# Kernel optimization log

Hardware: AMD Instinct MI355X
Metric: run time of the kernel (lower is better)

The kernel has to match this reference:

```python
import jax, jax.numpy as jnp
import numpy as np
from jax import lax

EPS = 1e-5


def _conv(x, w, b, stride, pad):
    # x: [B,C,H,W], w: [O,I,kh,kw] (NCHW / OIHW, same as torch Conv2d)
    y = lax.conv_general_dilated(
        x, w, window_strides=stride,
        padding=[(pad[0], pad[0]), (pad[1], pad[1])],
        dimension_numbers=('NCHW', 'OIHW', 'NCHW'))
    return y + b[None, :, None, None]


def _bn(x, gamma, beta, mean, var):
    # BatchNorm2d in eval mode (running statistics)
    inv = gamma / jnp.sqrt(var + EPS)
    return x * inv[None, :, None, None] + (beta - mean * inv)[None, :, None, None]


def _mask_time(x, lens):
    # Vectorized replacement of the per-sample narrow/fill loop:
    # zero every time step >= lens[b] along the last axis.
    t = jnp.arange(x.shape[3])
    keep = (t[None, :] < lens[:, None]).astype(x.dtype)  # [B, W]
    return x * keep[:, None, None, :]


def _new_len(lens, kernel_w, stride_w, pad_w):
    # matches get_new_sequence_lengths for Conv2d with dilation 1
    return (lens + 2 * pad_w - (kernel_w - 1) - 1) // stride_w + 1


def _forward(inputs, seq_lengths,
             w1, b1, g1, be1, m1, v1,
             w2, b2, g2, be2, m2, v2):
    lens = seq_lengths.astype(jnp.int32)
    # layer 1: Conv2d(1,32,(41,11),(2,2),(20,5))
    x = _conv(inputs, w1, b1, (2, 2), (20, 5))
    lens = _new_len(lens, 11, 2, 5)
    x = _mask_time(x, lens)
    # BatchNorm2d(32) -> mask
    x = _mask_time(_bn(x, g1, be1, m1, v1), lens)
    # Hardtanh(0,20) -> mask
    x = _mask_time(jnp.clip(x, 0.0, 20.0), lens)
    # layer 2: Conv2d(32,32,(21,11),(2,1),(10,5))
    x = _conv(x, w2, b2, (2, 1), (10, 5))
    lens = _new_len(lens, 11, 1, 5)
    x = _mask_time(x, lens)
    x = _mask_time(_bn(x, g2, be2, m2, v2), lens)
    x = _mask_time(jnp.clip(x, 0.0, 20.0), lens)
    return x, lens


def setup_inputs() -> dict:
    key = jax.random.key(0)
    ks = jax.random.split(key, 8)
    inputs = jax.random.normal(ks[0], (32, 1, 161, 1024), dtype=jnp.float32)
    seq_lengths = jax.random.randint(ks[1], (32,), 1, 1024, dtype=jnp.int32)
    w1 = jax.random.normal(ks[2], (32, 1, 41, 11), dtype=jnp.float32) * 0.05
    b1 = jax.random.normal(ks[3], (32,), dtype=jnp.float32) * 0.05
    w2 = jax.random.normal(ks[4], (32, 32, 21, 11), dtype=jnp.float32) * 0.02
    b2 = jax.random.normal(ks[5], (32,), dtype=jnp.float32) * 0.05
    g1 = jnp.ones((32,), jnp.float32)
    be1 = jnp.zeros((32,), jnp.float32)
    m1 = jax.random.normal(ks[6], (32,), dtype=jnp.float32) * 0.1
    v1 = jnp.ones((32,), jnp.float32)
    g2 = jnp.ones((32,), jnp.float32)
    be2 = jnp.zeros((32,), jnp.float32)
    m2 = jax.random.normal(ks[7], (32,), dtype=jnp.float32) * 0.1
    v2 = jnp.ones((32,), jnp.float32)
    return {"inputs": inputs, "seq_lengths": seq_lengths,
            "w1": w1, "b1": b1, "g1": g1, "be1": be1, "m1": m1, "v1": v1,
            "w2": w2, "b2": b2, "g2": g2, "be2": be2, "m2": m2, "v2": v2}


def reference(inputs, seq_lengths, w1, b1, g1, be1, m1, v1,
              w2, b2, g2, be2, m2, v2):
    return _forward(inputs, seq_lengths, w1, b1, g1, be1, m1, v1,
                    w2, b2, g2, be2, m2, v2)
```

## Files before the change

kernel.cpp:

```cpp
#include <hip/hip_runtime.h>
#include <math.h>

#define B_    32
#define H_IN  161
#define W_IN  1024
#define C1_   32
#define H1_   81
#define W1_   512
#define C2_   32
#define H2_   41
#define W2_   512

#define OUT_X_SZ ((size_t)B_ * C2_ * H2_ * W2_)

#define WF2_B    0u
#define WF1_B    473088u
#define SCSH_B   515072u
#define LENS1_B  515584u
#define XG_B     515712u

#define WF2_N    236544
#define WF1_N    20992

typedef __bf16 v8bf __attribute__((ext_vector_type(8)));
typedef float v16f __attribute__((ext_vector_type(16)));

static __device__ __forceinline__ unsigned short f2bf(float f) {
    unsigned int u = __float_as_uint(f);
    unsigned int r = (u + 0x7fffu + ((u >> 16) & 1u)) >> 16;
    return (unsigned short)r;
}

__global__ void prep_kernel(const float* __restrict__ w1, const float* __restrict__ b1,
                            const float* __restrict__ g1, const float* __restrict__ be1,
                            const float* __restrict__ m1, const float* __restrict__ v1,
                            const float* __restrict__ w2, const float* __restrict__ b2,
                            const float* __restrict__ g2, const float* __restrict__ be2,
                            const float* __restrict__ m2, const float* __restrict__ v2,
                            const int* __restrict__ lens,
                            unsigned short* __restrict__ wf1, unsigned short* __restrict__ wf2,
                            float* __restrict__ scsh, int* __restrict__ lens1,
                            float* __restrict__ out_lens)
{
    const int i = blockIdx.x * blockDim.x + threadIdx.x;
    const int stride = gridDim.x * blockDim.x;

    for (int idx = i; idx < WF2_N; idx += stride) {
        int j  = idx & 7;
        int l  = (idx >> 3) & 63;
        int f  = idx >> 9;
        int ch = f & 1;
        int kwkh = f >> 1;
        int kw = kwkh % 11;
        int kh = kwkh / 11;
        int oc = l & 31;
        int c  = ch * 16 + ((l >> 5) << 3) + j;
        wf2[idx] = f2bf(w2[((oc * 32 + c) * 21 + kh) * 11 + kw]);
    }
    for (int idx = i; idx < WF1_N; idx += stride) {
        int j  = idx & 7;
        int l  = (idx >> 3) & 63;
        int kh = idx >> 9;
        int k  = ((l >> 5) << 3) + j;
        int oc = l & 31;
        wf1[idx] = (k < 11) ? f2bf(w1[oc * 451 + kh * 11 + k]) : (unsigned short)0;
    }
    if (i < 32) {
        float s1 = g1[i] / sqrtf(v1[i] + 1e-5f);
        scsh[i]      = s1;
        scsh[32 + i] = b1[i] * s1 + be1[i] - m1[i] * s1;
        float s2 = g2[i] / sqrtf(v2[i] + 1e-5f);
        scsh[64 + i] = s2;
        scsh[96 + i] = b2[i] * s2 + be2[i] - m2[i] * s2;
        int l1 = (lens[i] - 1) / 2 + 1;
        if (l1 > W1_) l1 = W1_;
        lens1[i] = l1;
        out_lens[i] = (float)l1;
    }
}

__global__ __launch_bounds__(256) void conv1_mfma(
    const float* __restrict__ x,
    const unsigned short* __restrict__ wf1,
    const float* __restrict__ scsh,
    const int* __restrict__ lens1,
    unsigned short* __restrict__ xg)
{
    const int t    = threadIdx.x;
    const int lane = t & 63;
    const int l31  = lane & 31;
    const int lhi  = lane >> 5;
    const int wv   = t >> 6;
    const int w0   = blockIdx.x * 256;
    const int h    = blockIdx.y;
    const int b    = blockIdx.z;

    __shared__ unsigned int srow[2][264];

    v16f acc0, acc1;
#pragma unroll
    for (int i = 0; i < 16; ++i) { acc0[i] = 0.f; acc1[i] = 0.f; }

    const int r0 = 2 * h - 20;
    const int cb = 2 * w0 - 5;
    const float* xb = x + (size_t)b * (H_IN * W_IN);

    const int dwbase = wv * 64 + l31 + 4 * lhi;

    {
        float a0 = 0.f, a1 = 0.f, c0v = 0.f, c1v = 0.f;
        if (r0 >= 0 && r0 < H_IN) {
            const float* src = xb + (size_t)r0 * W_IN;
            int c0 = cb + 2 * t;
            if ((unsigned)c0 < (unsigned)W_IN)       a0 = src[c0];
            if ((unsigned)(c0 + 1) < (unsigned)W_IN) a1 = src[c0 + 1];
            if (t < 7) {
                int c1 = cb + 2 * (256 + t);
                if ((unsigned)c1 < (unsigned)W_IN)       c0v = src[c1];
                if ((unsigned)(c1 + 1) < (unsigned)W_IN) c1v = src[c1 + 1];
            }
        }
        srow[0][t] = (unsigned int)f2bf(a0) | ((unsigned int)f2bf(a1) << 16);
        if (t < 7)
            srow[0][256 + t] = (unsigned int)f2bf(c0v) | ((unsigned int)f2bf(c1v) << 16);
    }
    __syncthreads();

    for (int kh = 0; kh < 41; ++kh) {
        const int p = kh & 1;
        const int rn = r0 + kh + 1;
        const bool rv = (kh < 40) && (rn >= 0) && (rn < H_IN);

        float a0 = 0.f, a1 = 0.f, c0v = 0.f, c1v = 0.f;
        if (rv) {
            const float* src = xb + (size_t)rn * W_IN;
            int c0 = cb + 2 * t;
            if ((unsigned)c0 < (unsigned)W_IN)       a0 = src[c0];
            if ((unsigned)(c0 + 1) < (unsigned)W_IN) a1 = src[c0 + 1];
            if (t < 7) {
                int c1 = cb + 2 * (256 + t);
                if ((unsigned)c1 < (unsigned)W_IN)       c0v = src[c1];
                if ((unsigned)(c1 + 1) < (unsigned)W_IN) c1v = src[c1 + 1];
            }
        }

        const int r = r0 + kh;
        if (r >= 0 && r < H_IN) {
            uint4 a_u = *((const uint4*)wf1 + kh * 32 + lane);
            v8bf a = __builtin_bit_cast(v8bf, a_u);
            const unsigned int* bp = &srow[p][0];
            {
                int dw = dwbase;
                uint4 bu;
                bu.x = bp[dw]; bu.y = bp[dw + 1]; bu.z = bp[dw + 2]; bu.w = bp[dw + 3];
                v8bf bb = __builtin_bit_cast(v8bf, bu);
                acc0 = __builtin_amdgcn_mfma_f32_32x32x16_bf16(a, bb, acc0, 0, 0, 0);
            }
            {
                int dw = dwbase + 32;
                uint4 bu;
                bu.x = bp[dw]; bu.y = bp[dw + 1]; bu.z = bp[dw + 2]; bu.w = bp[dw + 3];
                v8bf bb = __builtin_bit_cast(v8bf, bu);
                acc1 = __builtin_amdgcn_mfma_f32_32x32x16_bf16(a, bb, acc1, 0, 0, 0);
            }
        }

        if (rv) {
            srow[p ^ 1][t] = (unsigned int)f2bf(a0) | ((unsigned int)f2bf(a1) << 16);
            if (t < 7)
                srow[p ^ 1][256 + t] = (unsigned int)f2bf(c0v) | ((unsigned int)f2bf(c1v) << 16);
        }
        __syncthreads();
    }

    const int l1 = lens1[b];
#pragma unroll
    for (int nt = 0; nt < 2; ++nt) {
        const int w = w0 + wv * 64 + nt * 32 + l31;
        const bool keep = (w < l1);
        unsigned short* dp = xg + (((size_t)b * H1_ + h) * W1_ + w) * 32;
#pragma unroll
        for (int rq = 0; rq < 4; ++rq) {
            unsigned int wd[2];
#pragma unroll
            for (int d = 0; d < 2; ++d) {
                int rg = rq * 4 + d * 2;
                int oc = 8 * rq + 4 * lhi + d * 2;
                float av0 = (nt == 0) ? acc0[rg]     : acc1[rg];
                float av1 = (nt == 0) ? acc0[rg + 1] : acc1[rg + 1];
                float v0 = fminf(fmaxf(fmaf(av0, scsh[oc],     scsh[32 + oc]), 0.f), 20.f);
                float v1 = fminf(fmaxf(fmaf(av1, scsh[oc + 1], scsh[33 + oc]), 0.f), 20.f);
                if (!keep) { v0 = 0.f; v1 = 0.f; }
                wd[d] = (unsigned int)f2bf(v0) | ((unsigned int)f2bf(v1) << 16);
            }
            uint2 u; u.x = wd[0]; u.y = wd[1];
            *(uint2*)(dp + 8 * rq + 4 * lhi) = u;
        }
    }
}

#define C2BUF 17024

__global__ __launch_bounds__(128, 2) void conv2_mfma(
    const unsigned short* __restrict__ xg,
    const unsigned short* __restrict__ wf2,
    const float* __restrict__ scsh,
    const int* __restrict__ lens1,
    float* __restrict__ out)
{
    const int t    = threadIdx.x;
    const int lane = t & 63;
    const int l31  = lane & 31;
    const int lhi  = lane >> 5;
    const int wid  = t >> 6;

    const int id   = blockIdx.x;
    const int sid  = (id & 7) * 168 + (id >> 3);
    const int wblk = sid & 1;
    const int bh   = sid >> 1;
    const int hp   = bh % 21;
    const int b    = bh / 21;
    const int h0   = hp << 1;
    const bool h1v = (h0 + 1) < 41;

    __shared__ __align__(16) char sbuf[2 * C2BUF];

    const int w0B = wblk << 8;
    const unsigned short* xb = xg + (size_t)b * (H1_ * W1_ * 32);

    int srcoff[9], ldsoff[9];
    bool vld[9];
#pragma unroll
    for (int i = 0; i < 9; ++i) {
        int k   = t + i * 128;
        int pos = k >> 2;
        int sg  = k & 3;
        int wp  = w0B + pos - 5;
        vld[i]    = (k < 1064) && (wp >= 0) && (wp < W1_);
        srcoff[i] = wp * 64 + sg * 16;
        ldsoff[i] = pos * 64 + ((sg ^ ((pos >> 1) & 3)) << 4);
    }

    const int rlo = max(0, 2 * h0 - 10);
    const int rhi = min(80, 2 * h0 + 12);

    v16f acc[2][4];
#pragma unroll
    for (int hh = 0; hh < 2; ++hh)
#pragma unroll
        for (int mt = 0; mt < 4; ++mt)
#pragma unroll
            for (int q = 0; q < 16; ++q) acc[hh][mt][q] = 0.f;

    uint4 g[9];

#define C2_STAGE_LOAD(ROW)                                                   \
    {                                                                        \
        const char* xrow = (const char*)(xb + (size_t)(ROW) * (W1_ * 32));   \
        _Pragma("unroll")                                                    \
        for (int i = 0; i < 9; ++i) {                                        \
            g[i].x = g[i].y = g[i].z = g[i].w = 0u;                          \
            if (vld[i]) g[i] = *(const uint4*)(xrow + srcoff[i]);            \
        }                                                                    \
    }

#define C2_STAGE_WRITE(PP)                                                   \
    {                                                                        \
        char* dst = sbuf + (PP) * C2BUF;                                     \
        _Pragma("unroll")                                                    \
        for (int i = 0; i < 8; ++i) *(uint4*)(dst + ldsoff[i]) = g[i];       \
        if (t < 40) *(uint4*)(dst + ldsoff[8]) = g[8];                       \
    }

    C2_STAGE_LOAD(rlo);
    C2_STAGE_WRITE(0);
    __syncthreads();

    const uint4* wq = (const uint4*)wf2;
    const int pbase = (wid << 7) + l31;

    for (int r = rlo; r <= rhi; ++r) {
        const int p = (r - rlo) & 1;

        if (r < rhi) C2_STAGE_LOAD(r + 1);

        const int kh0 = r + 10 - 2 * h0;
        const int kh1 = kh0 - 2;
        const bool vh0 = (kh0 <= 20);
        const bool vh1 = h1v && (kh1 >= 0);
        const int f0 = kh0 * 22;
        const int f1 = kh1 * 22;
        const char* bb = sbuf + p * C2BUF;

        __builtin_amdgcn_s_setprio(1);
#pragma unroll
        for (int kw = 0; kw < 11; ++kw) {
            const int pos0 = pbase + kw;
            const int swz  = (pos0 >> 1) & 3;
            const int a0   = (pos0 << 6) + ((lhi ^ swz) << 4);
            const int a1   = a0 ^ 32;
            uint4 b00 = *(const uint4*)(bb + a0);
            uint4 b01 = *(const uint4*)(bb + a0 + 2048);
            uint4 b02 = *(const uint4*)(bb + a0 + 4096);
            uint4 b03 = *(const uint4*)(bb + a0 + 6144);
            uint4 b10 = *(const uint4*)(bb + a1);
            uint4 b11 = *(const uint4*)(bb + a1 + 2048);
            uint4 b12 = *(const uint4*)(bb + a1 + 4096);
            uint4 b13 = *(const uint4*)(bb + a1 + 6144);
            if (vh0) {
                v8bf A0 = __builtin_bit_cast(v8bf, wq[(f0 + 2 * kw) * 64 + lane]);
                v8bf A1 = __builtin_bit_cast(v8bf, wq[(f0 + 2 * kw + 1) * 64 + lane]);
                acc[0][0] = __builtin_amdgcn_mfma_f32_32x32x16_bf16(A0, __builtin_bit_cast(v8bf, b00), acc[0][0], 0, 0, 0);
                acc[0][1] = __builtin_amdgcn_mfma_f32_32x32x16_bf16(A0, __builtin_bit_cast(v8bf, b01), acc[0][1], 0, 0, 0);
                acc[0][2] = __builtin_amdgcn_mfma_f32_32x32x16_bf16(A0, __builtin_bit_cast(v8bf, b02), acc[0][2], 0, 0, 0);
                acc[0][3] = __builtin_amdgcn_mfma_f32_32x32x16_bf16(A0, __builtin_bit_cast(v8bf, b03), acc[0][3], 0, 0, 0);
                acc[0][0] = __builtin_amdgcn_mfma_f32_32x32x16_bf16(A1, __builtin_bit_cast(v8bf, b10), acc[0][0], 0, 0, 0);
                acc[0][1] = __builtin_amdgcn_mfma_f32_32x32x16_bf16(A1, __builtin_bit_cast(v8bf, b11), acc[0][1], 0, 0, 0);
                acc[0][2] = __builtin_amdgcn_mfma_f32_32x32x16_bf16(A1, __builtin_bit_cast(v8bf, b12), acc[0][2], 0, 0, 0);
                acc[0][3] = __builtin_amdgcn_mfma_f32_32x32x16_bf16(A1, __builtin_bit_cast(v8bf, b13), acc[0][3], 0, 0, 0);
            }
            if (vh1) {
                v8bf C0 = __builtin_bit_cast(v8bf, wq[(f1 + 2 * kw) * 64 + lane]);
                v8bf C1 = __builtin_bit_cast(v8bf, wq[(f1 + 2 * kw + 1) * 64 + lane]);
                acc[1][0] = __builtin_amdgcn_mfma_f32_32x32x16_bf16(C0, __builtin_bit_cast(v8bf, b00), acc[1][0], 0, 0, 0);
                acc[1][1] = __builtin_amdgcn_mfma_f32_32x32x16_bf16(C0, __builtin_bit_cast(v8bf, b01), acc[1][1], 0, 0, 0);
                acc[1][2] = __builtin_amdgcn_mfma_f32_32x32x16_bf16(C0, __builtin_bit_cast(v8bf, b02), acc[1][2], 0, 0, 0);
                acc[1][3] = __builtin_amdgcn_mfma_f32_32x32x16_bf16(C0, __builtin_bit_cast(v8bf, b03), acc[1][3], 0, 0, 0);
                acc[1][0] = __builtin_amdgcn_mfma_f32_32x32x16_bf16(C1, __builtin_bit_cast(v8bf, b10), acc[1][0], 0, 0, 0);
                acc[1][1] = __builtin_amdgcn_mfma_f32_32x32x16_bf16(C1, __builtin_bit_cast(v8bf, b11), acc[1][1], 0, 0, 0);
                acc[1][2] = __builtin_amdgcn_mfma_f32_32x32x16_bf16(C1, __builtin_bit_cast(v8bf, b12), acc[1][2], 0, 0, 0);
                acc[1][3] = __builtin_amdgcn_mfma_f32_32x32x16_bf16(C1, __builtin_bit_cast(v8bf, b13), acc[1][3], 0, 0, 0);
            }
        }
        __builtin_amdgcn_s_setprio(0);

        if (r < rhi) C2_STAGE_WRITE(p ^ 1);
        __syncthreads();
    }

    const int l2 = lens1[b];
#pragma unroll
    for (int hh = 0; hh < 2; ++hh) {
        if (hh == 1 && !h1v) break;
        const int h = h0 + hh;
#pragma unroll
        for (int mt = 0; mt < 4; ++mt) {
            const int w = w0B + (wid << 7) + (mt << 5) + l31;
            const bool keep = (w < l2);
#pragma unroll
            for (int reg = 0; reg < 16; ++reg) {
                const int oc = (reg & 3) + 8 * (reg >> 2) + 4 * lhi;
                float v = fmaf(acc[hh][mt][reg], scsh[64 + oc], scsh[96 + oc]);
                v = fminf(fmaxf(v, 0.f), 20.f);
                out[(((size_t)b * C2_ + oc) * H2_ + h) * W2_ + w] = keep ? v : 0.f;
            }
        }
    }
}

extern "C" void kernel_launch(void* const* d_in, const int* in_sizes, int n_in,
                              void* d_out, int out_size, void* d_ws, size_t ws_size,
                              hipStream_t stream) {
    const float* inputs = (const float*)d_in[0];
    const int*   slen   = (const int*)d_in[1];
    const float* w1 = (const float*)d_in[2];
    const float* b1 = (const float*)d_in[3];
    const float* g1 = (const float*)d_in[4];
    const float* be1 = (const float*)d_in[5];
    const float* m1 = (const float*)d_in[6];
    const float* v1 = (const float*)d_in[7];
    const float* w2 = (const float*)d_in[8];
    const float* b2 = (const float*)d_in[9];
    const float* g2 = (const float*)d_in[10];
    const float* be2 = (const float*)d_in[11];
    const float* m2 = (const float*)d_in[12];
    const float* v2 = (const float*)d_in[13];

    char* ws = (char*)d_ws;
    unsigned short* wf2  = (unsigned short*)(ws + WF2_B);
    unsigned short* wf1  = (unsigned short*)(ws + WF1_B);
    float*          scsh = (float*)(ws + SCSH_B);
    int*            lens1 = (int*)(ws + LENS1_B);
    unsigned short* xg   = (unsigned short*)(ws + XG_B);

    float* out_x    = (float*)d_out;
    float* out_lens = out_x + OUT_X_SZ;

    hipLaunchKernelGGL(prep_kernel, dim3(256), dim3(256), 0, stream,
                       w1, b1, g1, be1, m1, v1, w2, b2, g2, be2, m2, v2,
                       slen, wf1, wf2, scsh, lens1, out_lens);

    hipLaunchKernelGGL(conv1_mfma, dim3(2, H1_, B_), dim3(256), 0, stream,
                       inputs, wf1, scsh, lens1, xg);

    hipLaunchKernelGGL(conv2_mfma, dim3(1344), dim3(128), 0, stream,
                       xg, wf2, scsh, lens1, out_x);
}
```

Baseline: 607.9 us.

## Use direct global-to-LDS loads in single-wave conv2 blocks without barriers

Conv2 now runs one wavefront per block, each covering 128 output columns instead of 256, with twice as many blocks. Input rows are staged with global_load_lds straight into a double-buffered LDS tile instead of going through registers. Because each block is a single wave, the __syncthreads barriers are dropped in favor of explicit s_waitcnt, and padded halo slots are zeroed by hand. This removes register staging and barrier cost. In exchange, the wider halo overhead loads more data per output, and ordering correctness rests on waitcnt semantics for LDS-DMA writes.

```diff
diff --git a/kernel.cpp b/kernel.cpp
--- a/kernel.cpp
+++ b/kernel.cpp
@@ -29,6 +29,13 @@
     unsigned int u = __float_as_uint(f);
     unsigned int r = (u + 0x7fffu + ((u >> 16) & 1u)) >> 16;
     return (unsigned short)r;
+}
+
+static __device__ __forceinline__ void gl_lds16(const void* g, void* l) {
+    __builtin_amdgcn_global_load_lds(
+        (const __attribute__((address_space(1))) unsigned int*)g,
+        (__attribute__((address_space(3))) unsigned int*)l,
+        16, 0, 0);
 }
 
 __global__ void prep_kernel(const float* __restrict__ w1, const float* __restrict__ b1,
@@ -199,47 +206,46 @@
     }
 }
 
-#define C2BUF 17024
-
-__global__ __launch_bounds__(128, 2) void conv2_mfma(
+#define C2POS 144
+#define C2BUF (C2POS * 64)
+
+__global__ __launch_bounds__(64, 2) void conv2_mfma(
     const unsigned short* __restrict__ xg,
     const unsigned short* __restrict__ wf2,
     const float* __restrict__ scsh,
     const int* __restrict__ lens1,
     float* __restrict__ out)
 {
-    const int t    = threadIdx.x;
-    const int lane = t & 63;
+    const int lane = threadIdx.x;
     const int l31  = lane & 31;
     const int lhi  = lane >> 5;
-    const int wid  = t >> 6;
-
-    const int id   = blockIdx.x;
-    const int sid  = (id & 7) * 168 + (id >> 3);
-    const int wblk = sid & 1;
-    const int bh   = sid >> 1;
-    const int hp   = bh % 21;
-    const int b    = bh / 21;
-    const int h0   = hp << 1;
+
+    const int id  = blockIdx.x;
+    const int sid = (id & 7) * 336 + (id >> 3);
+    const int qw  = sid & 3;
+    const int bh  = sid >> 2;
+    const int hp  = bh % 21;
+    const int b   = bh / 21;
+    const int h0  = hp << 1;
     const bool h1v = (h0 + 1) < 41;
 
     __shared__ __align__(16) char sbuf[2 * C2BUF];
 
-    const int w0B = wblk << 8;
+    const int wbase = qw << 7;
     const unsigned short* xb = xg + (size_t)b * (H1_ * W1_ * 32);
 
-    int srcoff[9], ldsoff[9];
-    bool vld[9];
+    int soff[9];
 #pragma unroll
     for (int i = 0; i < 9; ++i) {
-        int k   = t + i * 128;
-        int pos = k >> 2;
-        int sg  = k & 3;
-        int wp  = w0B + pos - 5;
-        vld[i]    = (k < 1064) && (wp >= 0) && (wp < W1_);
-        srcoff[i] = wp * 64 + sg * 16;
-        ldsoff[i] = pos * 64 + ((sg ^ ((pos >> 1) & 3)) << 4);
-    }
+        int k  = i * 64 + lane;
+        int P  = k >> 2;
+        int sg = (k & 3) ^ ((P >> 1) & 3);
+        int wp = wbase + P - 5;
+        bool v = (wp >= 0) && (wp < W1_);
+        soff[i] = (v ? wp * 64 : 0) + sg * 16;
+    }
+    const bool haszero = (qw == 0) || (qw == 3);
+    const int  zoff    = (((qw == 0 ? 0 : 133) + (lane >> 2)) << 6) + ((lane & 3) << 4);
 
     const int rlo = max(0, 2 * h0 - 10);
     const int rhi = min(80, 2 * h0 + 12);
@@ -252,37 +258,34 @@
 #pragma unroll
             for (int q = 0; q < 16; ++q) acc[hh][mt][q] = 0.f;
 
-    uint4 g[9];
-
-#define C2_STAGE_LOAD(ROW)                                                   \
-    {                                                                        \
-        const char* xrow = (const char*)(xb + (size_t)(ROW) * (W1_ * 32));   \
-        _Pragma("unroll")                                                    \
-        for (int i = 0; i < 9; ++i) {                                        \
-            g[i].x = g[i].y = g[i].z = g[i].w = 0u;                          \
-            if (vld[i]) g[i] = *(const uint4*)(xrow + srcoff[i]);            \
-        }                                                                    \
-    }
-
-#define C2_STAGE_WRITE(PP)                                                   \
-    {                                                                        \
-        char* dst = sbuf + (PP) * C2BUF;                                     \
-        _Pragma("unroll")                                                    \
-        for (int i = 0; i < 8; ++i) *(uint4*)(dst + ldsoff[i]) = g[i];       \
-        if (t < 40) *(uint4*)(dst + ldsoff[8]) = g[8];                       \
-    }
-
-    C2_STAGE_LOAD(rlo);
-    C2_STAGE_WRITE(0);
-    __syncthreads();
-
-    const uint4* wq = (const uint4*)wf2;
-    const int pbase = (wid << 7) + l31;
+    {
+        const char* xrow = (const char*)(xb + (size_t)rlo * (W1_ * 32));
+#pragma unroll
+        for (int i = 0; i < 9; ++i)
+            gl_lds16(xrow + soff[i], sbuf + i * 1024);
+    }
+
+    const uint4* wfq = (const uint4*)wf2;
 
     for (int r = rlo; r <= rhi; ++r) {
         const int p = (r - rlo) & 1;
-
-        if (r < rhi) C2_STAGE_LOAD(r + 1);
+        const char* bb = sbuf + p * C2BUF;
+
+        asm volatile("s_waitcnt vmcnt(0)" ::: "memory");
+
+        if (haszero && lane < 20) {
+            uint4 z; z.x = z.y = z.z = z.w = 0u;
+            *(uint4*)(const_cast<char*>(bb) + zoff) = z;
+        }
+
+        if (r < rhi) {
+            asm volatile("s_waitcnt lgkmcnt(0)" ::: "memory");
+            const char* xrow = (const char*)(xb + (size_t)(r + 1) * (W1_ * 32));
+            char* db = sbuf + (p ^ 1) * C2BUF;
+#pragma unroll
+            for (int i = 0; i < 9; ++i)
+                gl_lds16(xrow + soff[i], db + i * 1024);
+        }
 
         const int kh0 = r + 10 - 2 * h0;
         const int kh1 = kh0 - 2;
@@ -290,14 +293,13 @@
         const bool vh1 = h1v && (kh1 >= 0);
         const int f0 = kh0 * 22;
         const int f1 = kh1 * 22;
-        const char* bb = sbuf + p * C2BUF;
 
         __builtin_amdgcn_s_setprio(1);
 #pragma unroll
         for (int kw = 0; kw < 11; ++kw) {
-            const int pos0 = pbase + kw;
-            const int swz  = (pos0 >> 1) & 3;
-            const int a0   = (pos0 << 6) + ((lhi ^ swz) << 4);
+            const int P0   = l31 + kw;
+            const int swz  = (P0 >> 1) & 3;
+            const int a0   = (P0 << 6) + ((lhi ^ swz) << 4);
             const int a1   = a0 ^ 32;
             uint4 b00 = *(const uint4*)(bb + a0);
             uint4 b01 = *(const uint4*)(bb + a0 + 2048);
@@ -308,8 +310,8 @@
             uint4 b12 = *(const uint4*)(bb + a1 + 4096);
             uint4 b13 = *(const uint4*)(bb + a1 + 6144);
             if (vh0) {
-                v8bf A0 = __builtin_bit_cast(v8bf, wq[(f0 + 2 * kw) * 64 + lane]);
-                v8bf A1 = __builtin_bit_cast(v8bf, wq[(f0 + 2 * kw + 1) * 64 + lane]);
+                v8bf A0 = __builtin_bit_cast(v8bf, wfq[(f0 + 2 * kw) * 64 + lane]);
+                v8bf A1 = __builtin_bit_cast(v8bf, wfq[(f0 + 2 * kw + 1) * 64 + lane]);
                 acc[0][0] = __builtin_amdgcn_mfma_f32_32x32x16_bf16(A0, __builtin_bit_cast(v8bf, b00), acc[0][0], 0, 0, 0);
                 acc[0][1] = __builtin_amdgcn_mfma_f32_32x32x16_bf16(A0, __builtin_bit_cast(v8bf, b01), acc[0][1], 0, 0, 0);
                 acc[0][2] = __builtin_amdgcn_mfma_f32_32x32x16_bf16(A0, __builtin_bit_cast(v8bf, b02), acc[0][2], 0, 0, 0);
@@ -320,8 +322,8 @@
                 acc[0][3] = __builtin_amdgcn_mfma_f32_32x32x16_bf16(A1, __builtin_bit_cast(v8bf, b13), acc[0][3], 0, 0, 0);
             }
             if (vh1) {
-                v8bf C0 = __builtin_bit_cast(v8bf, wq[(f1 + 2 * kw) * 64 + lane]);
-                v8bf C1 = __builtin_bit_cast(v8bf, wq[(f1 + 2 * kw + 1) * 64 + lane]);
+                v8bf C0 = __builtin_bit_cast(v8bf, wfq[(f1 + 2 * kw) * 64 + lane]);
+                v8bf C1 = __builtin_bit_cast(v8bf, wfq[(f1 + 2 * kw + 1) * 64 + lane]);
                 acc[1][0] = __builtin_amdgcn_mfma_f32_32x32x16_bf16(C0, __builtin_bit_cast(v8bf, b00), acc[1][0], 0, 0, 0);
                 acc[1][1] = __builtin_amdgcn_mfma_f32_32x32x16_bf16(C0, __builtin_bit_cast(v8bf, b01), acc[1][1], 0, 0, 0);
                 acc[1][2] = __builtin_amdgcn_mfma_f32_32x32x16_bf16(C0, __builtin_bit_cast(v8bf, b02), acc[1][2], 0, 0, 0);
@@ -333,9 +335,6 @@
             }
         }
         __builtin_amdgcn_s_setprio(0);
-
-        if (r < rhi) C2_STAGE_WRITE(p ^ 1);
-        __syncthreads();
     }
 
     const int l2 = lens1[b];
@@ -345,7 +344,7 @@
         const int h = h0 + hh;
 #pragma unroll
         for (int mt = 0; mt < 4; ++mt) {
-            const int w = w0B + (wid << 7) + (mt << 5) + l31;
+            const int w = wbase + (mt << 5) + l31;
             const bool keep = (w < l2);
 #pragma unroll
             for (int reg = 0; reg < 16; ++reg) {
@@ -393,6 +392,6 @@
     hipLaunchKernelGGL(conv1_mfma, dim3(2, H1_, B_), dim3(256), 0, stream,
                        inputs, wf1, scsh, lens1, xg);
 
-    hipLaunchKernelGGL(conv2_mfma, dim3(1344), dim3(128), 0, stream,
+    hipLaunchKernelGGL(conv2_mfma, dim3(2688), dim3(64), 0, stream,
                        xg, wf2, scsh, lens1, out_x);
 }
```

Result: faster. 564.1 us (-7.2%).
